# Kernel optimization log

Measured on AMD Instinct MI355X. Metric: run time of the kernel, lower is better.

## Reference

```python
import jax, jax.numpy as jnp
import numpy as np

BETA = 0.25


def setup_inputs() -> dict:
    key = jax.random.key(0)
    k1, k2 = jax.random.split(key)
    x = jax.random.normal(k1, (32, 64, 64, 64), dtype=jnp.float32)   # [B, C, H, W]
    emb = jax.random.normal(k2, (1024, 64), dtype=jnp.float32)       # [K, C] codebook
    return {"x": x, "emb": emb}


def reference(x, emb):
    b, c, h, w = x.shape
    # (b h w) c
    z = jnp.transpose(x, (0, 2, 3, 1)).reshape(-1, c)
    # squared euclidean distances (argmin identical to torch.cdist argmin)
    # ||z||^2 - 2 z e^T + ||e||^2, never taking sqrt since only argmin is used
    d = (jnp.sum(z * z, axis=1, keepdims=True)
         - 2.0 * jnp.einsum('nc,kc->nk', z, emb)
         + jnp.sum(emb * emb, axis=1)[None, :])        # [N, K]
    idx = jnp.argmin(d, axis=1)                        # [N] int
    e = emb[idx]                                       # gather [N, C]
    e = jnp.transpose(e.reshape(b, h, w, c), (0, 3, 1, 2))  # [B, C, H, W]
    codebook_loss = jnp.mean((jax.lax.stop_gradient(x) - e) ** 2)
    commitment_loss = BETA * jnp.mean((x - jax.lax.stop_gradient(e)) ** 2)
    loss = codebook_loss + commitment_loss
    o = x + jax.lax.stop_gradient(e - x)               # straight-through
    indices = idx.reshape(b, h, w)
    return (o, loss, indices)
```

## Files before the change

### kernel.cpp

```cpp
#include <hip/hip_runtime.h>

#define BATCH   32
#define CCH     64
#define HW      4096
#define NPIX    (BATCH * HW)
#define KCODES  1024
#define NELEM   (NPIX * CCH)
#define MB      256
#define CK      128
#define NBLK    (NPIX / MB)
#define MARGIN_Q 4u
#define QSCALE   4096.0f
#define QBASE    1048576.0f

typedef _Float16 f16;
typedef __attribute__((ext_vector_type(8))) _Float16 f16x8;
typedef __attribute__((ext_vector_type(4))) float    f32x4;

static __device__ __forceinline__ f32x4 mfma16(f16x8 a, f16x8 b, f32x4 c) {
    return __builtin_amdgcn_mfma_f32_16x16x32_f16(a, b, c, 0, 0, 0);
}

static __device__ __forceinline__ void dma16(void* lds, const void* g) {
    __builtin_amdgcn_global_load_lds(
        (const __attribute__((address_space(1))) unsigned int*)g,
        (__attribute__((address_space(3))) unsigned int*)lds, 16, 0, 0);
}

static __device__ __forceinline__ unsigned med3u(unsigned a, unsigned b, unsigned c) {
    unsigned d;
    asm("v_med3_u32 %0, %1, %2, %3" : "=v"(d) : "v"(a), "v"(b), "v"(c));
    return d;
}

#define WS_EEB_F   64
#define WS_CBH_B   8192
#define WS_CBL_B   139264

__global__ __launch_bounds__(256) void vq_prep(
    const float* __restrict__ emb, float* __restrict__ wsf,
    unsigned* __restrict__ wsu, f16* __restrict__ cbH, f16* __restrict__ cbL,
    float* __restrict__ eeb_g)
{
    const int t   = threadIdx.x;
    const int gid = blockIdx.x * 256 + t;
    const int row = gid >> 3, gi = gid & 7;
    if (gid == 0) { wsf[0] = 0.f; wsu[2] = 0u; }
    const float* src = emb + (size_t)row * CCH + gi * 8;
    float4 v0 = *(const float4*)(src);
    float4 v1 = *(const float4*)(src + 4);
    float vv[8] = {v0.x, v0.y, v0.z, v0.w, v1.x, v1.y, v1.z, v1.w};
    f16x8 h, l;
    float s = 0.f;
#pragma unroll
    for (int j = 0; j < 8; ++j) {
        f16 hh = (f16)vv[j];
        h[j] = hh;
        l[j] = (f16)(vv[j] - (float)hh);
        s = fmaf(vv[j], vv[j], s);
    }
    const int off = row * 64 + 8 * (gi ^ (row & 7));
    *(f16x8*)(cbH + off) = h;
    *(f16x8*)(cbL + off) = l;
    s += __shfl_xor(s, 1, 64);
    s += __shfl_xor(s, 2, 64);
    s += __shfl_xor(s, 4, 64);
    if (gi == 0) eeb_g[row] = fmaf(s, QSCALE, QBASE);
}

__global__ __launch_bounds__(512, 4) void vq_main(
    const float* __restrict__ x,
    const float* __restrict__ emb,
    const f16* __restrict__ cbH, const f16* __restrict__ cbL,
    const float* __restrict__ eeb_g,
    float* __restrict__ o, float* __restrict__ idx_out,
    float* __restrict__ acc, unsigned* __restrict__ done,
    float* __restrict__ loss)
{
    __shared__ __align__(16) char smem[65536];
    __shared__ float eebl[2][CK];
    __shared__ unsigned bu1[MB], bu2[MB];
    __shared__ float wred[8];
    __shared__ unsigned short amb[MB];
    __shared__ int amb_n;
    __shared__ __align__(16) float zsh[CCH];
    __shared__ double rbd[8];
    __shared__ int rbi[8];

    const int t    = threadIdx.x;
    const int lane = t & 63;
    const int w    = t >> 6;
    const int col  = lane & 15;
    const int quad = lane >> 4;
    const int c7   = col & 7;
    const int sw0  = 8 * (quad ^ c7);
    const int sw1  = sw0 ^ 32;
    const int n0   = blockIdx.x * MB;
    const int b    = n0 >> 12;
    const int p0   = n0 & 4095;
    const float* xb = x + (size_t)b * (CCH * HW) + p0;

    auto stage = [&](int chunk, int bufi) {
        const int k0 = chunk * CK;
        char* lb = smem + bufi * 32768;
        const char* gH = (const char*)cbH + (size_t)k0 * 128 + w * 2048 + lane * 16;
        const char* gL = (const char*)cbL + (size_t)k0 * 128 + w * 2048 + lane * 16;
        char* lH = lb + w * 2048;
        char* lL = lb + 16384 + w * 2048;
        dma16(lH,        gH);
        dma16(lH + 1024, gH + 1024);
        dma16(lL,        gL);
        dma16(lL + 1024, gL + 1024);
        if (t < CK) eebl[bufi][t] = eeb_g[k0 + t];
    };

    stage(0, 0);

    f16x8 aH[2][2], aL[2][2];
#pragma unroll
    for (int rt = 0; rt < 2; ++rt) {
        const int pp = w * 32 + rt * 16 + col;
#pragma unroll
        for (int kc = 0; kc < 2; ++kc) {
            f16x8 h, l;
#pragma unroll
            for (int j = 0; j < 8; ++j) {
                const int c = kc * 32 + quad * 8 + j;
                float zs = -2.0f * xb[(size_t)c * HW + pp];
                f16 hh = (f16)zs;
                h[j] = hh;
                l[j] = (f16)(zs - (float)hh);
            }
            aH[rt][kc] = h;
            aL[rt][kc] = l;
        }
    }

    unsigned best[8], best2[8];
#pragma unroll
    for (int s = 0; s < 8; ++s) { best[s] = 0xFFFFFFFFu; best2[s] = 0xFFFFFFFFu; }

    const f32x4 zero4 = {0.f, 0.f, 0.f, 0.f};

    for (int chunk = 0; chunk < KCODES / CK; ++chunk) {
        const int cur = chunk & 1;
        __syncthreads();
        if (chunk + 1 < KCODES / CK) stage(chunk + 1, cur ^ 1);

        const f16* bufH = (const f16*)(smem + cur * 32768);
        const f16* bufL = bufH + 8192;
        const int k0 = chunk * CK;

#pragma unroll
        for (int tile = 0; tile < CK / 16; ++tile) {
            const f16* bh = bufH + (tile * 16 + col) * 64;
            const f16* bl = bufL + (tile * 16 + col) * 64;
            f16x8 bH0 = *(const f16x8*)(bh + sw0);
            f16x8 bH1 = *(const f16x8*)(bh + sw1);
            f16x8 bL0 = *(const f16x8*)(bl + sw0);
            f16x8 bL1 = *(const f16x8*)(bl + sw1);
            const float eebc = eebl[cur][tile * 16 + col];
            const unsigned kb = (unsigned)(k0 + tile * 16 + col);
#pragma unroll
            for (int rt = 0; rt < 2; ++rt) {
                f32x4 u = mfma16(aH[rt][0], bH0, zero4);
                f32x4 v = mfma16(aH[rt][1], bH1, zero4);
                u = mfma16(aL[rt][0], bH0, u);
                v = mfma16(aL[rt][1], bH1, v);
                u = mfma16(aH[rt][0], bL0, u);
                v = mfma16(aH[rt][1], bL1, v);
#pragma unroll
                for (int r = 0; r < 4; ++r) {
                    float uf = fmaf(u[r] + v[r], QSCALE, eebc);
                    unsigned pk = (((unsigned)uf) << 10) | kb;
                    const int s = rt * 4 + r;
                    const unsigned b0 = best[s];
                    best2[s] = med3u(b0, best2[s], pk);
                    best[s]  = min(b0, pk);
                }
            }
        }
    }

#pragma unroll
    for (int d = 1; d < 16; d <<= 1) {
#pragma unroll
        for (int s = 0; s < 8; ++s) {
            unsigned ob  = __shfl_xor(best[s],  d, 64);
            unsigned ob2 = __shfl_xor(best2[s], d, 64);
            best2[s] = min(min(best2[s], ob2), max(best[s], ob));
            best[s]  = min(best[s], ob);
        }
    }
    if (t == 0) amb_n = 0;
    if (col == 0) {
#pragma unroll
        for (int rt = 0; rt < 2; ++rt)
#pragma unroll
            for (int r = 0; r < 4; ++r) {
                const int pl = w * 32 + rt * 16 + quad * 4 + r;
                bu1[pl] = best[rt * 4 + r];
                bu2[pl] = best2[rt * 4 + r];
            }
    }
    __syncthreads();

    if (t < MB) {
        const unsigned qg = (bu2[t] >> 10) - (bu1[t] >> 10);
        if (qg < MARGIN_Q) {
            int p = atomicAdd(&amb_n, 1);
            amb[p] = (unsigned short)t;
        }
    }
    __syncthreads();
    const int na = amb_n;
    for (int i = 0; i < na; ++i) {
        const int pix = amb[i];
        if (t < CCH) zsh[t] = xb[(size_t)t * HW + pix];
        __syncthreads();
        double bd = 1e300; int bi = KCODES;
#pragma unroll 1
        for (int j = 0; j < 2; ++j) {
            const int k = t + j * 512;
            const float4* er4 = (const float4*)(emb + (size_t)k * CCH);
            const float4* zs4 = (const float4*)zsh;
            double d = 0.0;
#pragma unroll 1
            for (int c = 0; c < 16; ++c) {
                float4 ev = er4[c];
                float4 zv = zs4[c];
                double t0 = (double)zv.x - (double)ev.x;
                double t1 = (double)zv.y - (double)ev.y;
                double t2 = (double)zv.z - (double)ev.z;
                double t3 = (double)zv.w - (double)ev.w;
                d = fma(t0, t0, fma(t1, t1, fma(t2, t2, fma(t3, t3, d))));
            }
            if (d < bd) { bd = d; bi = k; }
        }
#pragma unroll 1
        for (int dlt = 1; dlt < 64; dlt <<= 1) {
            double od = __shfl_xor(bd, dlt, 64);
            int    oi = __shfl_xor(bi, dlt, 64);
            if (od < bd || (od == bd && oi < bi)) { bd = od; bi = oi; }
        }
        if (lane == 0) { rbd[w] = bd; rbi[w] = bi; }
        __syncthreads();
        if (t == 0) {
            double fb = rbd[0]; int fi = rbi[0];
            for (int q = 1; q < 8; ++q)
                if (rbd[q] < fb || (rbd[q] == fb && rbi[q] < fi)) { fb = rbd[q]; fi = rbi[q]; }
            bu1[pix] = (unsigned)fi;
        }
        __syncthreads();
    }

    const int pix  = t & 255;
    const int half = t >> 8;
    const unsigned bidx = bu1[pix] & 1023u;
    if (half == 0) {
        idx_out[n0 + pix] = (float)bidx;
    }
    float ss = 0.f;
    {
        const float4* er4 = (const float4*)(emb + (size_t)bidx * CCH) + half * 8;
        const float* xbt = xb + pix;
        float* ob = o + (size_t)b * (CCH * HW) + p0 + pix;
#pragma unroll
        for (int i = 0; i < 8; ++i) {
            float4 ev = er4[i];
            float evv[4] = {ev.x, ev.y, ev.z, ev.w};
#pragma unroll
            for (int q = 0; q < 4; ++q) {
                const int c = half * 32 + i * 4 + q;
                float xv = xbt[(size_t)c * HW];
                float e  = evv[q];
                ob[(size_t)c * HW] = xv + (e - xv);
                float d = xv - e;
                ss = fmaf(d, d, ss);
            }
        }
    }
    for (int off = 32; off; off >>= 1) ss += __shfl_down(ss, off, 64);
    if (lane == 0) wred[w] = ss;
    __syncthreads();
    if (t == 0) {
        float s2 = 0.f;
#pragma unroll
        for (int q = 0; q < 8; ++q) s2 += wred[q];
        float old = atomicAdd(acc, s2);
        asm volatile("" : : "v"(old));
        unsigned prev = atomicAdd(done, 1u);
        if (prev == (unsigned)(NBLK - 1)) {
            float a = atomicAdd(acc, 0.0f);
            *loss = 1.25f * a * (1.0f / (float)NELEM);
        }
    }
}

extern "C" void kernel_launch(void* const* d_in, const int* in_sizes, int n_in,
                              void* d_out, int out_size, void* d_ws, size_t ws_size,
                              hipStream_t stream) {
    const float* x   = (const float*)d_in[0];
    const float* emb = (const float*)d_in[1];
    float*    out = (float*)d_out;
    float*    wsf = (float*)d_ws;
    unsigned* wsu = (unsigned*)d_ws;
    char*     wsb = (char*)d_ws;

    float* o_out    = out;
    float* loss_out = out + NELEM;
    float* idx_out  = out + NELEM + 1;
    float* eeb_g    = wsf + WS_EEB_F;
    f16*   cbH      = (f16*)(wsb + WS_CBH_B);
    f16*   cbL      = (f16*)(wsb + WS_CBL_B);

    vq_prep<<<32, 256, 0, stream>>>(emb, wsf, wsu, cbH, cbL, eeb_g);
    vq_main<<<NBLK, 512, 0, stream>>>(x, emb, cbH, cbL, eeb_g, o_out,
                                      idx_out, wsf, wsu + 2, loss_out);
}
```

Baseline: 154.8 us.

## Track top-3 candidates and resolve two-way ties with cheap per-thread fp64 check

New measurement: 159.1 us. 2.8% more time.

```diff
diff --git a/kernel.cpp b/kernel.cpp
--- a/kernel.cpp
+++ b/kernel.cpp
@@ -9,7 +9,7 @@
 #define MB      256
 #define CK      128
 #define NBLK    (NPIX / MB)
-#define MARGIN_Q 4u
+#define MARGIN_Q 5u
 #define QSCALE   4096.0f
 #define QBASE    1048576.0f
 
@@ -79,10 +79,10 @@
 {
     __shared__ __align__(16) char smem[65536];
     __shared__ float eebl[2][CK];
-    __shared__ unsigned bu1[MB], bu2[MB];
+    __shared__ unsigned bu1[MB], bu2[MB], bu3[MB];
     __shared__ float wred[8];
-    __shared__ unsigned short amb[MB];
-    __shared__ int amb_n;
+    __shared__ unsigned short plist[MB], flist[MB];
+    __shared__ int np, nf;
     __shared__ __align__(16) float zsh[CCH];
     __shared__ double rbd[8];
     __shared__ int rbi[8];
@@ -136,9 +136,11 @@
         }
     }
 
-    unsigned best[8], best2[8];
-#pragma unroll
-    for (int s = 0; s < 8; ++s) { best[s] = 0xFFFFFFFFu; best2[s] = 0xFFFFFFFFu; }
+    unsigned best[8], best2[8], best3[8];
+#pragma unroll
+    for (int s = 0; s < 8; ++s) {
+        best[s] = 0xFFFFFFFFu; best2[s] = 0xFFFFFFFFu; best3[s] = 0xFFFFFFFFu;
+    }
 
     const f32x4 zero4 = {0.f, 0.f, 0.f, 0.f};
 
@@ -169,14 +171,17 @@
                 v = mfma16(aL[rt][1], bH1, v);
                 u = mfma16(aH[rt][0], bL0, u);
                 v = mfma16(aH[rt][1], bL1, v);
+                u = mfma16(aL[rt][0], bL0, u);
+                v = mfma16(aL[rt][1], bL1, v);
 #pragma unroll
                 for (int r = 0; r < 4; ++r) {
                     float uf = fmaf(u[r] + v[r], QSCALE, eebc);
                     unsigned pk = (((unsigned)uf) << 10) | kb;
                     const int s = rt * 4 + r;
-                    const unsigned b0 = best[s];
-                    best2[s] = med3u(b0, best2[s], pk);
-                    best[s]  = min(b0, pk);
+                    const unsigned b1 = best[s], b2 = best2[s];
+                    best3[s] = med3u(b2, best3[s], pk);
+                    best2[s] = med3u(b1, b2, pk);
+                    best[s]  = min(b1, pk);
                 }
             }
         }
@@ -186,13 +191,19 @@
     for (int d = 1; d < 16; d <<= 1) {
 #pragma unroll
         for (int s = 0; s < 8; ++s) {
-            unsigned ob  = __shfl_xor(best[s],  d, 64);
-            unsigned ob2 = __shfl_xor(best2[s], d, 64);
-            best2[s] = min(min(best2[s], ob2), max(best[s], ob));
-            best[s]  = min(best[s], ob);
-        }
-    }
-    if (t == 0) amb_n = 0;
+            unsigned o1 = __shfl_xor(best[s],  d, 64);
+            unsigned o2 = __shfl_xor(best2[s], d, 64);
+            unsigned o3 = __shfl_xor(best3[s], d, 64);
+            unsigned m1 = max(best[s], o1);
+            unsigned n2 = min(best2[s], o2);
+            unsigned x2 = max(best2[s], o2);
+            unsigned n3 = min(best3[s], o3);
+            best3[s] = min(min(max(m1, n2), x2), n3);
+            best2[s] = min(m1, n2);
+            best[s]  = min(best[s], o1);
+        }
+    }
+    if (t == 0) { np = 0; nf = 0; }
     if (col == 0) {
 #pragma unroll
         for (int rt = 0; rt < 2; ++rt)
@@ -201,21 +212,53 @@
                 const int pl = w * 32 + rt * 16 + quad * 4 + r;
                 bu1[pl] = best[rt * 4 + r];
                 bu2[pl] = best2[rt * 4 + r];
+                bu3[pl] = best3[rt * 4 + r];
             }
     }
     __syncthreads();
 
     if (t < MB) {
-        const unsigned qg = (bu2[t] >> 10) - (bu1[t] >> 10);
-        if (qg < MARGIN_Q) {
-            int p = atomicAdd(&amb_n, 1);
-            amb[p] = (unsigned short)t;
+        const unsigned q1 = bu1[t] >> 10;
+        if ((bu2[t] >> 10) - q1 < MARGIN_Q) {
+            if ((bu3[t] >> 10) - q1 < MARGIN_Q) {
+                flist[atomicAdd(&nf, 1)] = (unsigned short)t;
+            } else {
+                plist[atomicAdd(&np, 1)] = (unsigned short)t;
+            }
         }
     }
     __syncthreads();
-    const int na = amb_n;
-    for (int i = 0; i < na; ++i) {
-        const int pix = amb[i];
+
+    if (t < np) {
+        const int pix = plist[t];
+        const unsigned k1 = bu1[pix] & 1023u, k2 = bu2[pix] & 1023u;
+        const float* e1 = emb + (size_t)k1 * CCH;
+        const float* e2 = emb + (size_t)k2 * CCH;
+        const float* xp = xb + pix;
+        double d1 = 0.0, d2 = 0.0;
+#pragma unroll 1
+        for (int c = 0; c < CCH; c += 4) {
+            float4 a4 = *(const float4*)(e1 + c);
+            float4 b4 = *(const float4*)(e2 + c);
+            float xv0 = xp[(size_t)(c + 0) * HW];
+            float xv1 = xp[(size_t)(c + 1) * HW];
+            float xv2 = xp[(size_t)(c + 2) * HW];
+            float xv3 = xp[(size_t)(c + 3) * HW];
+            double ta0 = (double)xv0 - (double)a4.x, tb0 = (double)xv0 - (double)b4.x;
+            double ta1 = (double)xv1 - (double)a4.y, tb1 = (double)xv1 - (double)b4.y;
+            double ta2 = (double)xv2 - (double)a4.z, tb2 = (double)xv2 - (double)b4.z;
+            double ta3 = (double)xv3 - (double)a4.w, tb3 = (double)xv3 - (double)b4.w;
+            d1 = fma(ta0, ta0, fma(ta1, ta1, fma(ta2, ta2, fma(ta3, ta3, d1))));
+            d2 = fma(tb0, tb0, fma(tb1, tb1, fma(tb2, tb2, fma(tb3, tb3, d2))));
+        }
+        const unsigned kw = (d2 < d1 || (d2 == d1 && k2 < k1)) ? k2 : k1;
+        bu1[pix] = kw;
+    }
+
+    const int nfl = nf;
+    for (int i = 0; i < nfl; ++i) {
+        const int pix = flist[i];
+        __syncthreads();
         if (t < CCH) zsh[t] = xb[(size_t)t * HW + pix];
         __syncthreads();
         double bd = 1e300; int bi = KCODES;
@@ -251,8 +294,8 @@
                 if (rbd[q] < fb || (rbd[q] == fb && rbi[q] < fi)) { fb = rbd[q]; fi = rbi[q]; }
             bu1[pix] = (unsigned)fi;
         }
-        __syncthreads();
-    }
+    }
+    __syncthreads();
 
     const int pix  = t & 255;
     const int half = t >> 8;
```
